# Optimization experiments

Hardware: AMD Instinct MI355X
Metric: run time of the kernel (lower is better)

Reference implementation:

```python
import jax, jax.numpy as jnp
import numpy as np

EPS = 1e-12  # torch F.normalize eps
N, C, T = 16, 128, 16384
K, G = 64, 9  # clusters, ghost clusters


def setup_inputs() -> dict:
    key = jax.random.key(0)
    k1, k2, k3 = jax.random.split(key, 3)
    x = jax.random.normal(k1, (N, C, T), dtype=jnp.float32)
    conv_w = jax.random.normal(k2, (K + G, C), dtype=jnp.float32)  # 1x1 conv, no bias (vladv2=False)
    centroids = jax.random.uniform(k3, (K, C), dtype=jnp.float32)  # torch.rand init
    cluster_weights = jnp.ones((K,), dtype=jnp.float32)
    return {"x": x, "conv_w": conv_w, "centroids": centroids, "cluster_weights": cluster_weights}


def _l2norm(v, axis):
    return v / jnp.maximum(jnp.linalg.norm(v, axis=axis, keepdims=True), EPS)


def reference(x, conv_w, centroids, cluster_weights):
    # x: [N, C, T] (W=1 collapsed). Descriptor-wise L2 norm over channel dim.
    xn = _l2norm(x, axis=1)
    # 1x1 conv -> soft assignment logits over K+G clusters, softmax over all, keep K.
    logits = jnp.einsum('nct,kc->nkt', xn, conv_w)
    soft = jax.nn.softmax(logits, axis=1)[:, :K]  # [N, K, T]
    # VLAD: sum_t a_kt * (x_t - c_k) = (a @ x^T) - (sum_t a_kt) * c_k
    a_sum = soft.sum(axis=-1)  # [N, K]
    vlad = jnp.einsum('nkt,nct->nkc', soft, xn) - a_sum[..., None] * centroids[None]  # [N, K, C]
    # intra-normalization per cluster
    vlad = _l2norm(vlad, axis=2)
    # parametric normalization: L2-normalized cluster weights
    cw = cluster_weights / jnp.maximum(jnp.linalg.norm(cluster_weights), EPS)
    vlad = vlad * cw[None, :, None]
    v = vlad.reshape(vlad.shape[0], -1)  # [N, K*C]
    return _l2norm(v, axis=1)
```

## Files before the change

### kernel.cpp

```cpp
#include <hip/hip_runtime.h>
#include <math.h>

#define N_  16
#define C_  128
#define T_  16384
#define K_  64
#define KG_ 73
#define CT  512
#define EPSN 1e-12f
#define P1  72
#define P2  72

typedef __bf16 bf16x4v __attribute__((ext_vector_type(4)));
typedef __bf16 bf16x8v __attribute__((ext_vector_type(8)));
typedef float  f32x4v  __attribute__((ext_vector_type(4)));

#define MFMA(a, b, c) __builtin_amdgcn_mfma_f32_16x16x32_bf16((a), (b), (c), 0, 0, 0)

__global__ __launch_bounds__(256, 2)
void k_main(const float* __restrict__ x, const float* __restrict__ conv_w,
            float* __restrict__ gacc, float* __restrict__ gasum)
{
    __shared__ __align__(16) __bf16 xb[C_ * P1];
    __shared__ __align__(16) __bf16 st[K_ * P2];

    const int tid  = threadIdx.x;
    const int lane = tid & 63;
    const int wv   = __builtin_amdgcn_readfirstlane(tid >> 6);
    const int q    = lane >> 4;
    const int l15  = lane & 15;
    const int n    = blockIdx.x >> 5;
    const int t0   = (blockIdx.x & 31) * CT;

    bf16x8v wf[5][4];
#pragma unroll
    for (int nt = 0; nt < 5; ++nt) {
        const int row = min(16 * nt + l15, KG_ - 1);
#pragma unroll
        for (int ks = 0; ks < 4; ++ks) {
            const float* wp = conv_w + (size_t)row * C_ + 32 * ks + 8 * q;
            const float4 w0 = *(const float4*)wp;
            const float4 w1 = *(const float4*)(wp + 4);
            bf16x8v f;
            f[0] = (__bf16)w0.x; f[1] = (__bf16)w0.y; f[2] = (__bf16)w0.z; f[3] = (__bf16)w0.w;
            f[4] = (__bf16)w1.x; f[5] = (__bf16)w1.y; f[6] = (__bf16)w1.z; f[7] = (__bf16)w1.w;
            wf[nt][ks] = f;
        }
    }

    f32x4v acc2[8];
#pragma unroll
    for (int i = 0; i < 8; ++i) acc2[i] = (f32x4v){0.f, 0.f, 0.f, 0.f};
    float asum_acc[4] = {0.f, 0.f, 0.f, 0.f};

    const int cst = tid >> 4, t4 = tid & 15;
    const float* xbase = x + ((size_t)(n * C_ + cst)) * T_ + 4 * t4;

    float4 pf[8];
#pragma unroll
    for (int r = 0; r < 8; ++r)
        pf[r] = *(const float4*)(xbase + (size_t)r * 16 * T_ + t0);

    for (int it = 0; it < 8; ++it) {
#pragma unroll
        for (int r = 0; r < 8; ++r) {
            const int c  = cst + 16 * r;
            const int s8 = 8 * (((cst >> 3) + 2 * r) & 3);
            bf16x4v v = { (__bf16)pf[r].x, (__bf16)pf[r].y, (__bf16)pf[r].z, (__bf16)pf[r].w };
            *(bf16x4v*)&xb[c * P1 + ((4 * t4) ^ s8)] = v;
        }
        __syncthreads();

        if (it < 7) {
            const int tb = t0 + (it + 1) * 64;
#pragma unroll
            for (int r = 0; r < 8; ++r)
                pf[r] = *(const float4*)(xbase + (size_t)r * 16 * T_ + tb);
        }

        f32x4v acc1[5];
#pragma unroll
        for (int i = 0; i < 5; ++i) acc1[i] = (f32x4v){0.f, 0.f, 0.f, 0.f};
        f32x4v gr = (f32x4v){0.f, 0.f, 0.f, 0.f};

        const int tq = (16 * wv + l15) ^ (8 * q);
#pragma unroll
        for (int ks = 0; ks < 4; ++ks) {
            const __bf16* base = &xb[(32 * ks + 8 * q) * P1 + tq];
            bf16x8v af;
            af[0] = base[0 * P1]; af[1] = base[1 * P1];
            af[2] = base[2 * P1]; af[3] = base[3 * P1];
            af[4] = base[4 * P1]; af[5] = base[5 * P1];
            af[6] = base[6 * P1]; af[7] = base[7 * P1];
            gr = MFMA(af, af, gr);
#pragma unroll
            for (int nt = 0; nt < 5; ++nt)
                acc1[nt] = MFMA(af, wf[nt][ks], acc1[nt]);
        }

        float rn[4];
#pragma unroll
        for (int r = 0; r < 4; ++r) {
            const float ss = __int_as_float(
                __builtin_amdgcn_ds_bpermute((20 * q + r) << 2, __float_as_int(gr[r])));
            rn[r] = 1.f / fmaxf(sqrtf(ss), EPSN);
        }

        float e[5][4];
        float d[4] = {0.f, 0.f, 0.f, 0.f};
#pragma unroll
        for (int nt = 0; nt < 5; ++nt) {
            const bool valid = (16 * nt + l15) < KG_;
#pragma unroll
            for (int r = 0; r < 4; ++r) {
                const float ev = __expf(acc1[nt][r] * rn[r]);
                const float evm = valid ? ev : 0.f;
                e[nt][r] = evm;
                d[r] += evm;
            }
        }
#pragma unroll
        for (int r = 0; r < 4; ++r) {
            d[r] += __shfl_xor(d[r], 1);
            d[r] += __shfl_xor(d[r], 2);
            d[r] += __shfl_xor(d[r], 4);
            d[r] += __shfl_xor(d[r], 8);
            d[r] = 1.f / d[r];
        }

#pragma unroll
        for (int nt = 0; nt < 4; ++nt) {
            bf16x4v sv;
            float ap = 0.f;
#pragma unroll
            for (int r = 0; r < 4; ++r) {
                const float s = e[nt][r] * d[r];
                ap += s;
                sv[r] = (__bf16)(s * rn[r]);
            }
            asum_acc[nt] += ap;
            *(bf16x4v*)&st[(16 * nt + l15) * P2 + 16 * wv + 4 * q] = sv;
        }
        __syncthreads();

        bf16x8v sa0 = *(const bf16x8v*)&st[(16 * wv + l15) * P2 +      8 * q];
        bf16x8v sa1 = *(const bf16x8v*)&st[(16 * wv + l15) * P2 + 32 + 8 * q];
#pragma unroll
        for (int nt2 = 0; nt2 < 8; ++nt2) {
            const int c = 16 * nt2 + l15;
            const int s = (2 * nt2 + (l15 >> 3)) & 3;
            const bf16x8v xf0 = *(const bf16x8v*)&xb[c * P1 +      8 * (q ^ s)];
            const bf16x8v xf1 = *(const bf16x8v*)&xb[c * P1 + 32 + 8 * (q ^ s)];
            acc2[nt2] = MFMA(sa0, xf0, acc2[nt2]);
            acc2[nt2] = MFMA(sa1, xf1, acc2[nt2]);
        }
        __syncthreads();
    }

#pragma unroll
    for (int nt2 = 0; nt2 < 8; ++nt2)
#pragma unroll
        for (int r = 0; r < 4; ++r)
            atomicAdd(&gacc[((size_t)n * K_ + (16 * wv + 4 * q + r)) * C_ + 16 * nt2 + l15],
                      acc2[nt2][r]);

#pragma unroll
    for (int nt = 0; nt < 4; ++nt) {
        float v = asum_acc[nt];
        v += __shfl_xor(v, 16);
        v += __shfl_xor(v, 32);
        if (q == 0) atomicAdd(&gasum[n * K_ + 16 * nt + l15], v);
    }
}

__global__ __launch_bounds__(64)
void k_post(const float* __restrict__ gacc, const float* __restrict__ gasum,
            const float* __restrict__ centroids, const float* __restrict__ cwv,
            float* __restrict__ out, float* __restrict__ nsq)
{
    const int b = blockIdx.x;
    const int n = b >> 6, k = b & 63;
    const int lane = threadIdx.x;

    const float cv = cwv[lane];
    float cs = cv * cv;
#pragma unroll
    for (int off = 32; off; off >>= 1) cs += __shfl_xor(cs, off);
    const float cwn = cwv[k] / fmaxf(sqrtf(cs), EPSN);

    const float asum = gasum[n * K_ + k];
    const float* ga = gacc + ((size_t)n * K_ + k) * C_;
    const float* ce = centroids + (size_t)k * C_;
    const float v0 = ga[lane]      - asum * ce[lane];
    const float v1 = ga[lane + 64] - asum * ce[lane + 64];
    float ss = v0 * v0 + v1 * v1;
#pragma unroll
    for (int off = 32; off; off >>= 1) ss += __shfl_xor(ss, off);
    const float scale = cwn / fmaxf(sqrtf(ss), EPSN);

    float* o = out + (size_t)n * (K_ * C_) + (size_t)k * C_;
    o[lane]      = v0 * scale;
    o[lane + 64] = v1 * scale;
    if (lane == 0) atomicAdd(&nsq[n], ss * scale * scale);
}

__global__ __launch_bounds__(256)
void k_norm(float* __restrict__ out, const float* __restrict__ nsq)
{
    const int i = blockIdx.x * 256 + threadIdx.x;
    const int n = i >> 13;
    const float r = 1.f / fmaxf(sqrtf(nsq[n]), EPSN);
    out[i] *= r;
}

extern "C" void kernel_launch(void* const* d_in, const int* in_sizes, int n_in,
                              void* d_out, int out_size, void* d_ws, size_t ws_size,
                              hipStream_t stream)
{
    const float* x         = (const float*)d_in[0];
    const float* conv_w    = (const float*)d_in[1];
    const float* centroids = (const float*)d_in[2];
    const float* cweights  = (const float*)d_in[3];
    float* out = (float*)d_out;

    float* gacc  = (float*)d_ws;
    float* gasum = gacc + N_ * K_ * C_;
    float* nsq   = gasum + N_ * K_;
    const size_t zbytes = (size_t)(N_ * K_ * C_ + N_ * K_ + N_) * sizeof(float);

    hipMemsetAsync(d_ws, 0, zbytes, stream);
    hipLaunchKernelGGL(k_main, dim3(N_ * (T_ / CT)), dim3(256), 0, stream,
                       x, conv_w, gacc, gasum);
    hipLaunchKernelGGL(k_post, dim3(N_ * K_), dim3(64), 0, stream,
                       gacc, gasum, centroids, cweights, out, nsq);
    hipLaunchKernelGGL(k_norm, dim3(N_ * K_ * C_ / 256), dim3(256), 0, stream,
                       out, nsq);
}
```

Measured before the change: 229.3 us.

## Double-buffer LDS tiles, read MFMA A-operand from global, replace atomics with partials

The x and soft-assignment tiles are double-buffered in LDS, which removes one barrier per iteration. The first GEMM's A fragments are now loaded as strided scalar reads straight from global memory instead of from the swizzled LDS tile. The second GEMM is retiled so each wave computes a 32-cluster by 64-channel block. The global float atomics and the memset of the accumulator are replaced by per-chunk partial sums that k_post reduces. The trade-offs are many uncoalesced global scalar loads, possible LDS bank conflicts from dropping the XOR swizzle, and extra partial-buffer traffic in k_post.

```diff
diff --git a/kernel.cpp b/kernel.cpp
--- a/kernel.cpp
+++ b/kernel.cpp
@@ -7,6 +7,7 @@
 #define K_  64
 #define KG_ 73
 #define CT  512
+#define NCH 32
 #define EPSN 1e-12f
 #define P1  72
 #define P2  72
@@ -19,18 +20,20 @@
 
 __global__ __launch_bounds__(256, 2)
 void k_main(const float* __restrict__ x, const float* __restrict__ conv_w,
-            float* __restrict__ gacc, float* __restrict__ gasum)
-{
-    __shared__ __align__(16) __bf16 xb[C_ * P1];
-    __shared__ __align__(16) __bf16 st[K_ * P2];
+            float* __restrict__ gaccp, float* __restrict__ gasump)
+{
+    __shared__ __align__(16) __bf16 xb[2][C_ * P1];
+    __shared__ __align__(16) __bf16 st[2][K_ * P2];
+    __shared__ float asq[4 * K_];
 
     const int tid  = threadIdx.x;
     const int lane = tid & 63;
     const int wv   = __builtin_amdgcn_readfirstlane(tid >> 6);
     const int q    = lane >> 4;
     const int l15  = lane & 15;
-    const int n    = blockIdx.x >> 5;
-    const int t0   = (blockIdx.x & 31) * CT;
+    const int n     = blockIdx.x >> 5;
+    const int chunk = blockIdx.x & 31;
+    const int t0    = chunk * CT;
 
     bf16x8v wf[5][4];
 #pragma unroll
@@ -56,20 +59,20 @@
     const int cst = tid >> 4, t4 = tid & 15;
     const float* xbase = x + ((size_t)(n * C_ + cst)) * T_ + 4 * t4;
 
+    const float* g1 = x + ((size_t)(n * C_ + 8 * q)) * T_ + t0 + 16 * wv + l15;
+
     float4 pf[8];
 #pragma unroll
     for (int r = 0; r < 8; ++r)
         pf[r] = *(const float4*)(xbase + (size_t)r * 16 * T_ + t0);
 
+    int p = 0;
     for (int it = 0; it < 8; ++it) {
 #pragma unroll
         for (int r = 0; r < 8; ++r) {
-            const int c  = cst + 16 * r;
-            const int s8 = 8 * (((cst >> 3) + 2 * r) & 3);
             bf16x4v v = { (__bf16)pf[r].x, (__bf16)pf[r].y, (__bf16)pf[r].z, (__bf16)pf[r].w };
-            *(bf16x4v*)&xb[c * P1 + ((4 * t4) ^ s8)] = v;
-        }
-        __syncthreads();
+            *(bf16x4v*)&xb[p][(cst + 16 * r) * P1 + 4 * t4] = v;
+        }
 
         if (it < 7) {
             const int tb = t0 + (it + 1) * 64;
@@ -83,15 +86,12 @@
         for (int i = 0; i < 5; ++i) acc1[i] = (f32x4v){0.f, 0.f, 0.f, 0.f};
         f32x4v gr = (f32x4v){0.f, 0.f, 0.f, 0.f};
 
-        const int tq = (16 * wv + l15) ^ (8 * q);
 #pragma unroll
         for (int ks = 0; ks < 4; ++ks) {
-            const __bf16* base = &xb[(32 * ks + 8 * q) * P1 + tq];
+            const float* gp = g1 + ((size_t)(32 * ks)) * T_ + it * 64;
             bf16x8v af;
-            af[0] = base[0 * P1]; af[1] = base[1 * P1];
-            af[2] = base[2 * P1]; af[3] = base[3 * P1];
-            af[4] = base[4 * P1]; af[5] = base[5 * P1];
-            af[6] = base[6 * P1]; af[7] = base[7 * P1];
+#pragma unroll
+            for (int j = 0; j < 8; ++j) af[j] = (__bf16)gp[(size_t)j * T_];
             gr = MFMA(af, af, gr);
 #pragma unroll
             for (int nt = 0; nt < 5; ++nt)
@@ -114,9 +114,8 @@
 #pragma unroll
             for (int r = 0; r < 4; ++r) {
                 const float ev = __expf(acc1[nt][r] * rn[r]);
-                const float evm = valid ? ev : 0.f;
-                e[nt][r] = evm;
-                d[r] += evm;
+                e[nt][r] = valid ? ev : 0.f;
+                d[r] += e[nt][r];
             }
         }
 #pragma unroll
@@ -139,42 +138,65 @@
                 sv[r] = (__bf16)(s * rn[r]);
             }
             asum_acc[nt] += ap;
-            *(bf16x4v*)&st[(16 * nt + l15) * P2 + 16 * wv + 4 * q] = sv;
+            *(bf16x4v*)&st[p][(16 * nt + l15) * P2 + 16 * wv + 4 * q] = sv;
         }
         __syncthreads();
 
-        bf16x8v sa0 = *(const bf16x8v*)&st[(16 * wv + l15) * P2 +      8 * q];
-        bf16x8v sa1 = *(const bf16x8v*)&st[(16 * wv + l15) * P2 + 32 + 8 * q];
-#pragma unroll
-        for (int nt2 = 0; nt2 < 8; ++nt2) {
-            const int c = 16 * nt2 + l15;
-            const int s = (2 * nt2 + (l15 >> 3)) & 3;
-            const bf16x8v xf0 = *(const bf16x8v*)&xb[c * P1 +      8 * (q ^ s)];
-            const bf16x8v xf1 = *(const bf16x8v*)&xb[c * P1 + 32 + 8 * (q ^ s)];
-            acc2[nt2] = MFMA(sa0, xf0, acc2[nt2]);
-            acc2[nt2] = MFMA(sa1, xf1, acc2[nt2]);
-        }
-        __syncthreads();
-    }
-
-#pragma unroll
-    for (int nt2 = 0; nt2 < 8; ++nt2)
-#pragma unroll
-        for (int r = 0; r < 4; ++r)
-            atomicAdd(&gacc[((size_t)n * K_ + (16 * wv + 4 * q + r)) * C_ + 16 * nt2 + l15],
-                      acc2[nt2][r]);
+        {
+            const int clp = wv >> 1;
+            const int chh = wv & 1;
+            bf16x8v sa[2][2];
+#pragma unroll
+            for (int clb = 0; clb < 2; ++clb)
+#pragma unroll
+                for (int ks2 = 0; ks2 < 2; ++ks2)
+                    sa[clb][ks2] = *(const bf16x8v*)
+                        &st[p][(16 * (2 * clp + clb) + l15) * P2 + 32 * ks2 + 8 * q];
+#pragma unroll
+            for (int cb = 0; cb < 4; ++cb) {
+                const int c = 16 * (4 * chh + cb) + l15;
+                const bf16x8v xf0 = *(const bf16x8v*)&xb[p][c * P1 + 8 * q];
+                const bf16x8v xf1 = *(const bf16x8v*)&xb[p][c * P1 + 32 + 8 * q];
+                acc2[cb]     = MFMA(sa[0][0], xf0, acc2[cb]);
+                acc2[cb]     = MFMA(sa[0][1], xf1, acc2[cb]);
+                acc2[4 + cb] = MFMA(sa[1][0], xf0, acc2[4 + cb]);
+                acc2[4 + cb] = MFMA(sa[1][1], xf1, acc2[4 + cb]);
+            }
+        }
+        p ^= 1;
+    }
+
+    {
+        const int clp = wv >> 1, chh = wv & 1;
+        float* gp = gaccp + ((size_t)(n * NCH + chunk) * K_) * C_;
+#pragma unroll
+        for (int clb = 0; clb < 2; ++clb)
+#pragma unroll
+            for (int cb = 0; cb < 4; ++cb)
+#pragma unroll
+                for (int r = 0; r < 4; ++r) {
+                    const int cl = 16 * (2 * clp + clb) + 4 * q + r;
+                    const int c  = 16 * (4 * chh + cb) + l15;
+                    gp[cl * C_ + c] = acc2[clb * 4 + cb][r];
+                }
+    }
 
 #pragma unroll
     for (int nt = 0; nt < 4; ++nt) {
         float v = asum_acc[nt];
         v += __shfl_xor(v, 16);
         v += __shfl_xor(v, 32);
-        if (q == 0) atomicAdd(&gasum[n * K_ + 16 * nt + l15], v);
+        if (q == 0) asq[wv * K_ + 16 * nt + l15] = v;
+    }
+    __syncthreads();
+    if (tid < K_) {
+        const float s = asq[tid] + asq[K_ + tid] + asq[2 * K_ + tid] + asq[3 * K_ + tid];
+        gasump[(n * NCH + chunk) * K_ + tid] = s;
     }
 }
 
 __global__ __launch_bounds__(64)
-void k_post(const float* __restrict__ gacc, const float* __restrict__ gasum,
+void k_post(const float* __restrict__ gaccp, const float* __restrict__ gasump,
             const float* __restrict__ centroids, const float* __restrict__ cwv,
             float* __restrict__ out, float* __restrict__ nsq)
 {
@@ -188,11 +210,20 @@
     for (int off = 32; off; off >>= 1) cs += __shfl_xor(cs, off);
     const float cwn = cwv[k] / fmaxf(sqrtf(cs), EPSN);
 
-    const float asum = gasum[n * K_ + k];
-    const float* ga = gacc + ((size_t)n * K_ + k) * C_;
+    float v0 = 0.f, v1 = 0.f;
+    const float* gp = gaccp + ((size_t)(n * NCH) * K_ + k) * C_;
+    for (int ch = 0; ch < NCH; ++ch) {
+        v0 += gp[lane];
+        v1 += gp[lane + 64];
+        gp += K_ * C_;
+    }
+    float asum = 0.f;
+    const float* gs = gasump + (size_t)(n * NCH) * K_ + k;
+    for (int ch = 0; ch < NCH; ++ch) asum += gs[ch * K_];
+
     const float* ce = centroids + (size_t)k * C_;
-    const float v0 = ga[lane]      - asum * ce[lane];
-    const float v1 = ga[lane + 64] - asum * ce[lane + 64];
+    v0 -= asum * ce[lane];
+    v1 -= asum * ce[lane + 64];
     float ss = v0 * v0 + v1 * v1;
 #pragma unroll
     for (int off = 32; off; off >>= 1) ss += __shfl_xor(ss, off);
@@ -223,16 +254,15 @@
     const float* cweights  = (const float*)d_in[3];
     float* out = (float*)d_out;
 
-    float* gacc  = (float*)d_ws;
-    float* gasum = gacc + N_ * K_ * C_;
-    float* nsq   = gasum + N_ * K_;
-    const size_t zbytes = (size_t)(N_ * K_ * C_ + N_ * K_ + N_) * sizeof(float);
-
-    hipMemsetAsync(d_ws, 0, zbytes, stream);
-    hipLaunchKernelGGL(k_main, dim3(N_ * (T_ / CT)), dim3(256), 0, stream,
-                       x, conv_w, gacc, gasum);
+    float* nsq    = (float*)d_ws;
+    float* gasump = nsq + 16;
+    float* gaccp  = gasump + N_ * NCH * K_;
+
+    hipMemsetAsync(nsq, 0, N_ * sizeof(float), stream);
+    hipLaunchKernelGGL(k_main, dim3(N_ * NCH), dim3(256), 0, stream,
+                       x, conv_w, gaccp, gasump);
     hipLaunchKernelGGL(k_post, dim3(N_ * K_), dim3(64), 0, stream,
-                       gacc, gasum, centroids, cweights, out, nsq);
+                       gaccp, gasump, centroids, cweights, out, nsq);
     hipLaunchKernelGGL(k_norm, dim3(N_ * K_ * C_ / 256), dim3(256), 0, stream,
                        out, nsq);
 }
```

Result: no change. 228.1 us (-0.5%).
